# Optimization experiments

Hardware: AMD Instinct MI355X
Metric: run time of the kernel (lower is better)

Reference implementation:

```python
import jax, jax.numpy as jnp
import numpy as np

B, D = 16384, 2048

def setup_inputs() -> dict:
    key = jax.random.key(0)
    k1, k2, k3 = jax.random.split(key, 3)
    x = jax.random.normal(k1, (B, D), dtype=jnp.float32)
    x_dot = jax.random.normal(k2, (B, D), dtype=jnp.float32)
    # linear score_fn weight, scaled like standard init
    W = jax.random.normal(k3, (D, D), dtype=jnp.float32) / np.sqrt(D).astype(np.float32)
    return {"x": x, "x_dot": x_dot, "W": W}


def reference(x, x_dot, W) -> jnp.ndarray:
    # score_fn: s = x @ W^T  -> [B, D]
    s = jnp.einsum('bd,ed->be', x, W)
    # G = I - s s^T / (1 + ||s||^2); kinetic = x_dot^T G x_dot.
    # Exact algebraic collapse (Sherman-Morrison rank-1 form):
    #   x_dot.G.x_dot = ||x_dot||^2 - (s.x_dot)^2 / (1 + ||s||^2)
    norm_sq = jnp.sum(s * s, axis=1)            # [B]
    sx = jnp.sum(s * x_dot, axis=1)             # [B]
    xx = jnp.sum(x_dot * x_dot, axis=1)         # [B]
    return xx - (sx * sx) / (1.0 + norm_sq)      # [B]
```

## Files before the change

### kernel.cpp

```cpp
#include <hip/hip_runtime.h>


#define MTOT 16384
#define DTOT 2048
#define NK 16

typedef unsigned char u8;
typedef __attribute__((ext_vector_type(4))) float f32x4;
typedef __attribute__((ext_vector_type(8))) int i32x8;

__device__ __forceinline__ unsigned f2e2m1(float f) {
    unsigned sgn = f < 0.f ? 8u : 0u;
    float a = fabsf(f);
    unsigned c;
    if      (a < 0.25f) c = 0;
    else if (a < 0.75f) c = 1;
    else if (a < 1.25f) c = 2;
    else if (a < 1.75f) c = 3;
    else if (a < 2.5f)  c = 4;
    else if (a < 3.5f)  c = 5;
    else if (a < 5.0f)  c = 6;
    else                c = 7;
    return sgn | c;
}

__device__ __forceinline__ void gload_lds16(const void* gptr, void* ldsptr) {
    __builtin_amdgcn_global_load_lds(
        (const __attribute__((address_space(1))) unsigned int*)gptr,
        (__attribute__((address_space(3))) unsigned int*)ldsptr,
        16, 0, 0);
}

#define BARS()   __builtin_amdgcn_s_barrier()
#define SCHED0() __builtin_amdgcn_sched_barrier(0)
#define LGKM0()  asm volatile("s_waitcnt lgkmcnt(0)")
#define WAITV(n) asm volatile("s_waitcnt vmcnt(" #n ")")

__global__ void cast4_kernel(const float* __restrict__ src, unsigned* __restrict__ dst,
                             int n8, float mul) {
    int stride = gridDim.x * blockDim.x;
    for (int i = blockIdx.x * blockDim.x + threadIdx.x; i < n8; i += stride) {
        f32x4 v0 = ((const f32x4*)src)[2 * (size_t)i];
        f32x4 v1 = ((const f32x4*)src)[2 * (size_t)i + 1];
        dst[i] =  f2e2m1(v0[0] * mul)        | (f2e2m1(v0[1] * mul) << 4)  |
                 (f2e2m1(v0[2] * mul) << 8)  | (f2e2m1(v0[3] * mul) << 12) |
                 (f2e2m1(v1[0] * mul) << 16) | (f2e2m1(v1[1] * mul) << 20) |
                 (f2e2m1(v1[2] * mul) << 24) | (f2e2m1(v1[3] * mul) << 28);
    }
}

__global__ __launch_bounds__(256, 4)
void gemmf4(const u8* __restrict__ xq, const u8* __restrict__ wq,
            const float* __restrict__ xdot,
            float* __restrict__ ns_acc, float* __restrict__ sx_acc,
            float* __restrict__ xx_acc) {
    __shared__ u8 lds[32768];

    const int tid  = threadIdx.x;
    const int lane = tid & 63;
    const int wid  = tid >> 6;
    const int wr = wid >> 1, wc = wid & 1;
    const int fr = lane & 15, fq = lane >> 4;

    const int bid = blockIdx.x;
    const int o   = (bid & 7) * 256 + (bid >> 3);
    const int brow = (o & 127) * 128;
    const int bcol = (o >> 7) * 128;

    const int RS = DTOT / 2;

    auto stage_region = [&](const u8* src, int region) {
#pragma unroll
        for (int c2 = 0; c2 < 2; ++c2) {
            const int c = c2 * 256 + tid;
            const int L = c >> 3, p = c & 7;
            const int q = p ^ (L & 7);
            gload_lds16(src + (size_t)(2 * L + (q >> 2)) * RS + (q & 3) * 16,
                        (char*)lds + region + c * 16);
        }
    };
    auto stage_tile = [&](int kt, int bufbyte) {
        const int kb = kt * 64;
        stage_region(xq + (size_t)brow * RS + kb, bufbyte);
        stage_region(wq + (size_t)bcol * RS + kb, bufbyte + 8192);
    };

    auto rdfrag = [&](int region, int row) -> int4 {
        const int L = row >> 1;
        const int p = ((((row & 1) << 2) | fq) ^ (L & 7));
        return *(const int4*)((const char*)lds + region + L * 128 + (p << 4));
    };
    auto mk8 = [](int4 v) -> i32x8 {
        i32x8 r;
        r[0] = v.x; r[1] = v.y; r[2] = v.z; r[3] = v.w;
        r[4] = 0;   r[5] = 0;   r[6] = 0;   r[7] = 0;
        return r;
    };

    f32x4 acc[4][4] = {};
    int4 bf[4], a0, a1;

    stage_tile(0, 0);
    WAITV(0);
    SCHED0(); BARS();

    for (int t = 0; t < NK; ++t) {
        const int buf   = (t & 1) * 16384;
        const int abase = buf;
        const int bbase = buf + 8192;

        {
            const int v = t + 1 > NK - 1 ? NK - 1 : t + 1;
            stage_tile(v, (~t & 1) * 16384);
        }

#pragma unroll
        for (int n = 0; n < 4; ++n) bf[n] = rdfrag(bbase, wc * 64 + n * 16 + fr);
        a0 = rdfrag(abase, wr * 64 + fr);
#pragma unroll
        for (int m = 0; m < 4; ++m) {
            if (m + 1 < 4) a1 = rdfrag(abase, wr * 64 + (m + 1) * 16 + fr);
            __builtin_amdgcn_s_setprio(1);
#pragma unroll
            for (int n = 0; n < 4; ++n)
                acc[m][n] = __builtin_amdgcn_mfma_scale_f32_16x16x128_f8f6f4(
                    mk8(a0), mk8(bf[n]), acc[m][n],
                    4, 4,
                    0, 0x7f7f7f7f,
                    0, 0x7f7f7f7f);
            __builtin_amdgcn_s_setprio(0);
            a0 = a1;
        }
        LGKM0();
        WAITV(0);
        SCHED0(); BARS();
    }

#pragma unroll
    for (int m = 0; m < 4; ++m) {
#pragma unroll
        for (int jj = 0; jj < 4; ++jj) {
            const int row = brow + wr * 64 + m * 16 + fq * 4 + jj;
            const float* xp = xdot + (size_t)row * DTOT + bcol + wc * 64 + fr;
            float pns = 0.f, psx = 0.f, pxx = 0.f;
#pragma unroll
            for (int n = 0; n < 4; ++n) {
                float s  = acc[m][n][jj];
                float xv = xp[n * 16];
                pns += s * s; psx += s * xv; pxx += xv * xv;
            }
#pragma unroll
            for (int msk = 1; msk < 16; msk <<= 1) {
                pns += __shfl_xor(pns, msk);
                psx += __shfl_xor(psx, msk);
                pxx += __shfl_xor(pxx, msk);
            }
            if (fr == 0) {
                atomicAdd(&ns_acc[row], pns);
                atomicAdd(&sx_acc[row], psx);
                atomicAdd(&xx_acc[row], pxx);
            }
        }
    }
}

__global__ void finalize_k(const float* __restrict__ ns, const float* __restrict__ sx,
                           const float* __restrict__ xx, float* __restrict__ out) {
    int i = blockIdx.x * blockDim.x + threadIdx.x;
    if (i < MTOT) out[i] = xx[i] - (sx[i] * sx[i]) / (4096.0f + ns[i]);
}

extern "C" void kernel_launch(void* const* d_in, const int* in_sizes, int n_in,
                              void* d_out, int out_size, void* d_ws, size_t ws_size,
                              hipStream_t stream) {
    const float* x  = (const float*)d_in[0];
    const float* xd = (const float*)d_in[1];
    const float* W  = (const float*)d_in[2];
    float* out = (float*)d_out;

    const size_t xq_bytes = (size_t)MTOT * DTOT / 2;
    const size_t wq_bytes = (size_t)DTOT * DTOT / 2;
    const size_t acc_bytes = (size_t)3 * MTOT * 4;

    u8* xq = (u8*)d_ws;
    u8* wq = (u8*)((char*)d_ws + xq_bytes);
    float* accs = (float*)((char*)d_ws + xq_bytes + wq_bytes);
    float* nsA = accs;
    float* sxA = accs + MTOT;
    float* xxA = accs + 2 * MTOT;
    (void)ws_size; (void)in_sizes; (void)n_in; (void)out_size;

    hipMemsetAsync(accs, 0, acc_bytes, stream);

    cast4_kernel<<<2048, 256, 0, stream>>>(x, (unsigned*)xq, MTOT * DTOT / 8, 1.0f);
    cast4_kernel<<<512, 256, 0, stream>>>(W, (unsigned*)wq, DTOT * DTOT / 8, 64.0f);
    gemmf4<<<2048, 256, 0, stream>>>(xq, wq, xd, nsA, sxA, xxA);
    finalize_k<<<MTOT / 256, 256, 0, stream>>>(nsA, sxA, xxA, out);
}
```

Before: 125.3 us.

## Shrink GEMM tiles to 64x64 and merge the two cast kernels

Reduces the FP4 GEMM block tile from 128x128 to 64x64. That quadruples the grid to 8192 blocks, halves LDS per block and raises the launch-bounds occupancy hint to 6. It also fuses the x and W FP4 cast kernels into one launch to save a kernel launch. The smaller tiles reuse each loaded operand less, so global/L2 traffic for the GEMM operands and xdot epilogue atomics per element increase. In exchange the change is meant to gain occupancy and latency hiding.

```diff
diff --git a/kernel.cpp b/kernel.cpp
--- a/kernel.cpp
+++ b/kernel.cpp
@@ -36,25 +36,29 @@
 #define LGKM0()  asm volatile("s_waitcnt lgkmcnt(0)")
 #define WAITV(n) asm volatile("s_waitcnt vmcnt(" #n ")")
 
-__global__ void cast4_kernel(const float* __restrict__ src, unsigned* __restrict__ dst,
-                             int n8, float mul) {
+__global__ void cast4two_kernel(const float* __restrict__ x, const float* __restrict__ W,
+                                unsigned* __restrict__ xq, unsigned* __restrict__ wq,
+                                int nx8, int ntot8) {
     int stride = gridDim.x * blockDim.x;
-    for (int i = blockIdx.x * blockDim.x + threadIdx.x; i < n8; i += stride) {
-        f32x4 v0 = ((const f32x4*)src)[2 * (size_t)i];
-        f32x4 v1 = ((const f32x4*)src)[2 * (size_t)i + 1];
-        dst[i] =  f2e2m1(v0[0] * mul)        | (f2e2m1(v0[1] * mul) << 4)  |
-                 (f2e2m1(v0[2] * mul) << 8)  | (f2e2m1(v0[3] * mul) << 12) |
-                 (f2e2m1(v1[0] * mul) << 16) | (f2e2m1(v1[1] * mul) << 20) |
-                 (f2e2m1(v1[2] * mul) << 24) | (f2e2m1(v1[3] * mul) << 28);
+    for (int i = blockIdx.x * blockDim.x + threadIdx.x; i < ntot8; i += stride) {
+        const float* s; unsigned* d; int j; float mul;
+        if (i < nx8) { s = x; d = xq; j = i; mul = 1.0f; }
+        else         { s = W; d = wq; j = i - nx8; mul = 64.0f; }
+        f32x4 v0 = ((const f32x4*)s)[2 * (size_t)j];
+        f32x4 v1 = ((const f32x4*)s)[2 * (size_t)j + 1];
+        d[j] =  f2e2m1(v0[0] * mul)        | (f2e2m1(v0[1] * mul) << 4)  |
+               (f2e2m1(v0[2] * mul) << 8)  | (f2e2m1(v0[3] * mul) << 12) |
+               (f2e2m1(v1[0] * mul) << 16) | (f2e2m1(v1[1] * mul) << 20) |
+               (f2e2m1(v1[2] * mul) << 24) | (f2e2m1(v1[3] * mul) << 28);
     }
 }
 
-__global__ __launch_bounds__(256, 4)
+__global__ __launch_bounds__(256, 6)
 void gemmf4(const u8* __restrict__ xq, const u8* __restrict__ wq,
             const float* __restrict__ xdot,
             float* __restrict__ ns_acc, float* __restrict__ sx_acc,
             float* __restrict__ xx_acc) {
-    __shared__ u8 lds[32768];
+    __shared__ u8 lds[16384];
 
     const int tid  = threadIdx.x;
     const int lane = tid & 63;
@@ -63,26 +67,19 @@
     const int fr = lane & 15, fq = lane >> 4;
 
     const int bid = blockIdx.x;
-    const int o   = (bid & 7) * 256 + (bid >> 3);
-    const int brow = (o & 127) * 128;
-    const int bcol = (o >> 7) * 128;
+    const int o   = (bid & 7) * 1024 + (bid >> 3);
+    const int brow = (o & 255) * 64;
+    const int bcol = (o >> 8) * 64;
 
     const int RS = DTOT / 2;
 
-    auto stage_region = [&](const u8* src, int region) {
-#pragma unroll
-        for (int c2 = 0; c2 < 2; ++c2) {
-            const int c = c2 * 256 + tid;
-            const int L = c >> 3, p = c & 7;
-            const int q = p ^ (L & 7);
-            gload_lds16(src + (size_t)(2 * L + (q >> 2)) * RS + (q & 3) * 16,
-                        (char*)lds + region + c * 16);
-        }
-    };
+    const int sL = tid >> 3, sp = tid & 7;
+    const int sq = sp ^ (sL & 7);
+    const size_t soff = (size_t)(2 * sL + (sq >> 2)) * RS + (sq & 3) * 16;
     auto stage_tile = [&](int kt, int bufbyte) {
         const int kb = kt * 64;
-        stage_region(xq + (size_t)brow * RS + kb, bufbyte);
-        stage_region(wq + (size_t)bcol * RS + kb, bufbyte + 8192);
+        gload_lds16(xq + (size_t)brow * RS + kb + soff, (char*)lds + bufbyte + tid * 16);
+        gload_lds16(wq + (size_t)bcol * RS + kb + soff, (char*)lds + bufbyte + 4096 + tid * 16);
     };
 
     auto rdfrag = [&](int region, int row) -> int4 {
@@ -97,54 +94,52 @@
         return r;
     };
 
-    f32x4 acc[4][4] = {};
-    int4 bf[4], a0, a1;
+    f32x4 acc[2][2] = {};
+    int4 af[2], bf[2];
 
     stage_tile(0, 0);
     WAITV(0);
     SCHED0(); BARS();
 
     for (int t = 0; t < NK; ++t) {
-        const int buf   = (t & 1) * 16384;
+        const int buf   = (t & 1) * 8192;
         const int abase = buf;
-        const int bbase = buf + 8192;
+        const int bbase = buf + 4096;
 
         {
             const int v = t + 1 > NK - 1 ? NK - 1 : t + 1;
-            stage_tile(v, (~t & 1) * 16384);
+            stage_tile(v, (~t & 1) * 8192);
         }
 
 #pragma unroll
-        for (int n = 0; n < 4; ++n) bf[n] = rdfrag(bbase, wc * 64 + n * 16 + fr);
-        a0 = rdfrag(abase, wr * 64 + fr);
+        for (int n = 0; n < 2; ++n) bf[n] = rdfrag(bbase, wc * 32 + n * 16 + fr);
 #pragma unroll
-        for (int m = 0; m < 4; ++m) {
-            if (m + 1 < 4) a1 = rdfrag(abase, wr * 64 + (m + 1) * 16 + fr);
-            __builtin_amdgcn_s_setprio(1);
+        for (int m = 0; m < 2; ++m) af[m] = rdfrag(abase, wr * 32 + m * 16 + fr);
+        __builtin_amdgcn_s_setprio(1);
 #pragma unroll
-            for (int n = 0; n < 4; ++n)
+        for (int m = 0; m < 2; ++m)
+#pragma unroll
+            for (int n = 0; n < 2; ++n)
                 acc[m][n] = __builtin_amdgcn_mfma_scale_f32_16x16x128_f8f6f4(
-                    mk8(a0), mk8(bf[n]), acc[m][n],
+                    mk8(af[m]), mk8(bf[n]), acc[m][n],
                     4, 4,
                     0, 0x7f7f7f7f,
                     0, 0x7f7f7f7f);
-            __builtin_amdgcn_s_setprio(0);
-            a0 = a1;
-        }
+        __builtin_amdgcn_s_setprio(0);
         LGKM0();
         WAITV(0);
         SCHED0(); BARS();
     }
 
 #pragma unroll
-    for (int m = 0; m < 4; ++m) {
+    for (int m = 0; m < 2; ++m) {
 #pragma unroll
         for (int jj = 0; jj < 4; ++jj) {
-            const int row = brow + wr * 64 + m * 16 + fq * 4 + jj;
-            const float* xp = xdot + (size_t)row * DTOT + bcol + wc * 64 + fr;
+            const int row = brow + wr * 32 + m * 16 + fq * 4 + jj;
+            const float* xp = xdot + (size_t)row * DTOT + bcol + wc * 32 + fr;
             float pns = 0.f, psx = 0.f, pxx = 0.f;
 #pragma unroll
-            for (int n = 0; n < 4; ++n) {
+            for (int n = 0; n < 2; ++n) {
                 float s  = acc[m][n][jj];
                 float xv = xp[n * 16];
                 pns += s * s; psx += s * xv; pxx += xv * xv;
@@ -192,8 +187,9 @@
 
     hipMemsetAsync(accs, 0, acc_bytes, stream);
 
-    cast4_kernel<<<2048, 256, 0, stream>>>(x, (unsigned*)xq, MTOT * DTOT / 8, 1.0f);
-    cast4_kernel<<<512, 256, 0, stream>>>(W, (unsigned*)wq, DTOT * DTOT / 8, 64.0f);
-    gemmf4<<<2048, 256, 0, stream>>>(xq, wq, xd, nsA, sxA, xxA);
+    const int nx8 = MTOT * DTOT / 8, nw8 = DTOT * DTOT / 8;
+    cast4two_kernel<<<2048, 256, 0, stream>>>(x, W, (unsigned*)xq, (unsigned*)wq,
+                                              nx8, nx8 + nw8);
+    gemmf4<<<8192, 256, 0, stream>>>(xq, wq, xd, nsA, sxA, xxA);
     finalize_k<<<MTOT / 256, 256, 0, stream>>>(nsA, sxA, xxA, out);
 }
```

After: 173.8 us. 1.39x slower.
